# Performance work log

Measured on AMD Instinct MI355X. Metric: run time of the kernel, lower is better.

The kernel has to match this reference:

```python
import jax, jax.numpy as jnp
import numpy as np

BATCH, DIN, HID = 32768, 64, 1024


def setup_inputs() -> dict:
    key = jax.random.key(0)
    ks = jax.random.split(key, 8)
    s_in = 1.0 / np.sqrt(DIN)
    s_h = 1.0 / np.sqrt(HID)
    return {
        "z": jax.random.normal(ks[0], (BATCH, DIN), dtype=jnp.float32),
        # Hamiltonian net: DIN -> HID -> HID -> 1
        "W1": jax.random.normal(ks[1], (DIN, HID), dtype=jnp.float32) * s_in,
        "b1": jnp.zeros((HID,), jnp.float32),
        "W2": jax.random.normal(ks[2], (HID, HID), dtype=jnp.float32) * s_h,
        "b2": jnp.zeros((HID,), jnp.float32),
        "W3": jax.random.normal(ks[3], (HID, 1), dtype=jnp.float32) * s_h,
        "b3": jnp.zeros((1,), jnp.float32),
        # Forcing net: DIN -> HID -> DIN
        "Wf1": jax.random.normal(ks[4], (DIN, HID), dtype=jnp.float32) * s_in,
        "bf1": jnp.zeros((HID,), jnp.float32),
        "Wf2": jax.random.normal(ks[5], (HID, DIN), dtype=jnp.float32) * s_h,
        "bf2": jnp.zeros((DIN,), jnp.float32),
    }


def reference(z, W1, b1, W2, b2, W3, b3, Wf1, bf1, Wf2, bf2):
    def H_sum(zz):
        h1 = jnp.tanh(zz @ W1 + b1)          # [B, HID]
        h2 = jnp.tanh(h1 @ W2 + b2)          # [B, HID]
        return jnp.sum(h2 @ W3 + b3)         # scalar (sum of H over batch)

    gradH = jax.grad(H_sum)(z)               # [B, DIN]
    dim = z.shape[1] // 2
    # symplectic combine: dq/dt = dH/dp, dp/dt = -dH/dq
    hnn_term = jnp.concatenate([gradH[:, dim:], -gradH[:, :dim]], axis=-1)
    forcing_term = jnp.tanh(z @ Wf1 + bf1) @ Wf2 + bf2  # [B, DIN]
    return hnn_term + forcing_term
```

## Files before the change

### kernel.cpp

```cpp
#include <hip/hip_runtime.h>


typedef __attribute__((ext_vector_type(8))) short s16x8;
typedef __attribute__((ext_vector_type(4))) float f32x4;
typedef unsigned short u16;

#define DEVFN static __device__ __forceinline__

constexpr int DIN = 64;
constexpr int HID = 1024;

DEVFN u16 f2bf(float f) {
  unsigned u = __builtin_bit_cast(unsigned, f);
  u += 0x7fffu + ((u >> 16) & 1u);
  return (u16)(u >> 16);
}
DEVFN float bf2f(u16 h) {
  unsigned u = ((unsigned)h) << 16;
  return __builtin_bit_cast(float, u);
}
DEVFN float fast_tanh(float x) {
  float e = __builtin_amdgcn_exp2f(x * 2.8853900817779268f);
  return 1.0f - 2.0f * __builtin_amdgcn_rcpf(e + 1.0f);
}
DEVFN f32x4 mfma16(s16x8 a, s16x8 b, f32x4 c) {
  return __builtin_amdgcn_mfma_f32_16x16x32_bf16(a, b, c, 0, 0, 0);
}

#define GLOAD16(g, l) __builtin_amdgcn_global_load_lds( \
    (const __attribute__((address_space(1))) unsigned int*)(const void*)(g), \
    (__attribute__((address_space(3))) unsigned int*)(void*)(l), 16, 0, 0)

__global__ __launch_bounds__(256) void k0_prep(
    const float* __restrict__ W2, const float* __restrict__ W1,
    const float* __restrict__ Wf1, const float* __restrict__ Wf2,
    u16* __restrict__ W2tp, u16* __restrict__ W2c,
    u16* __restrict__ W1p, u16* __restrict__ Wf1p,
    u16* __restrict__ W1s, u16* __restrict__ Wf2p) {
  __shared__ u16 tl[64 * 65];
  const int bi = blockIdx.x >> 4, bj = blockIdx.x & 15;
  const int tid = threadIdx.x;
#pragma unroll
  for (int i = 0; i < 16; ++i) {
    int idx = i * 256 + tid;
    int r = idx >> 6, c = idx & 63;
    float v = W2[(size_t)(bi * 64 + r) * 1024 + bj * 64 + c];
    u16 b = f2bf(v);
    W2c[(size_t)(bi * 64 + r) * 1024 + bj * 64 + c] = b;
    tl[r * 65 + c] = b;
  }
  __syncthreads();
#pragma unroll
  for (int i = 0; i < 16; ++i) {
    int idx = i * 256 + tid;
    int r = idx >> 6, c = idx & 63;
    W2tp[(size_t)(bj * 64 + r) * 1024 + bi * 64 + c] = tl[c * 65 + r];
  }
  int id = blockIdx.x * 256 + tid;
  int n = id >> 6, k = id & 63;
  W1p[id]  = f2bf(W1[k * HID + n]);
  Wf1p[id] = f2bf(Wf1[k * HID + n]);
  int nn = id >> 10, kk2 = id & 1023;
  float s = (nn < 32) ? 1.f : -1.f;
  W1s[id]  = f2bf(s * W1[((nn + 32) & 63) * HID + kk2]);
  Wf2p[id] = f2bf(Wf2[kk2 * DIN + nn]);
}

__global__ __launch_bounds__(256) void k1_h1(const float* z, const u16* Wp,
                                             const float* b, u16* o) {
  __shared__ __align__(16) u16 zl[64 * 72];
  const int tid = threadIdx.x;
  const int lane = tid & 63, w = tid >> 6;
  const int nb = blockIdx.x & 7, mb = blockIdx.x >> 3;
  const size_t m0 = (size_t)mb * 64;
  const int n0 = nb * 128;
#pragma unroll
  for (int c = 0; c < 4; ++c) {
    int i4 = c * 256 + tid;
    int row = i4 >> 4, col4 = (i4 & 15) * 4;
    f32x4 v = *reinterpret_cast<const f32x4*>(z + (m0 + row) * DIN + col4);
    u16* d = zl + row * 72 + col4;
    d[0] = f2bf(v[0]); d[1] = f2bf(v[1]); d[2] = f2bf(v[2]); d[3] = f2bf(v[3]);
  }
  __syncthreads();
  f32x4 acc[8] = {};
#pragma unroll
  for (int kk = 0; kk < 2; ++kk) {
    const int karr = kk * 32 + ((lane >> 4) << 3);
    s16x8 a = *reinterpret_cast<const s16x8*>(zl + (16 * w + (lane & 15)) * 72 + karr);
#pragma unroll
    for (int fn = 0; fn < 8; ++fn) {
      int n = n0 + fn * 16 + (lane & 15);
      s16x8 bb = *reinterpret_cast<const s16x8*>(Wp + (size_t)n * 64 + karr);
      acc[fn] = mfma16(a, bb, acc[fn]);
    }
  }
#pragma unroll
  for (int fn = 0; fn < 8; ++fn) {
    int n = n0 + fn * 16 + (lane & 15);
    float bias = b[n];
#pragma unroll
    for (int j = 0; j < 4; ++j) {
      size_t m = m0 + 16 * w + ((lane >> 4) << 2) + j;
      o[m * HID + n] = f2bf(fast_tanh(acc[fn][j] + bias));
    }
  }
}

template <int MODE>
__global__ __launch_bounds__(512, 2) void k23_gemm(
    const u16* __restrict__ A, const u16* __restrict__ Bp,
    const float* __restrict__ b2, const float* __restrict__ W3,
    const u16* __restrict__ h1in, u16* __restrict__ outb) {
  extern __shared__ u16 lds[];
  const int tid = threadIdx.x;
  const int lane = tid & 63, w = tid >> 6;
  const int wr = w >> 2, wc = w & 3;
  const int xcd = blockIdx.x & 7, local = blockIdx.x >> 3;
  const size_t m0 = (size_t)(xcd * 16 + (local >> 2)) * 256;
  const int n0 = (local & 3) * 256;

  const u16* gpa[4]; const u16* gpb[4]; int lo[4];
#pragma unroll
  for (int c = 0; c < 4; ++c) {
    int idx = c * 512 + tid, row = idx >> 3, cg = idx & 7;
    int sc = (cg ^ (row & 7)) << 3;
    gpa[c] = A + (m0 + row) * 1024 + sc;
    gpb[c] = Bp + (size_t)(n0 + row) * 1024 + sc;
    lo[c] = idx * 8;
  }
#define STAGE_A(B_, T_) { _Pragma("unroll") for (int c = 0; c < 4; ++c) \
    GLOAD16(gpa[c] + (T_) * 64, lds + (B_) * 32768 + lo[c]); }
#define STAGE_B(B_, T_) { _Pragma("unroll") for (int c = 0; c < 4; ++c) \
    GLOAD16(gpb[c] + (T_) * 64, lds + (B_) * 32768 + 16384 + lo[c]); }

  const int swz = (lane & 7) << 3;
  int aoff[8], boff[4];
#pragma unroll
  for (int i = 0; i < 8; ++i)
    aoff[i] = (wr * 128 + i * 16 + (lane & 15)) * 64 + ((lane >> 4) << 3);
#pragma unroll
  for (int j = 0; j < 4; ++j)
    boff[j] = (wc * 64 + j * 16 + (lane & 15)) * 64 + ((lane >> 4) << 3);

  f32x4 acc[8][4] = {};

#define PHASE(B_, KK_) { \
    s16x8 af[8], bf[4]; \
    _Pragma("unroll") for (int i = 0; i < 8; ++i) \
      af[i] = *reinterpret_cast<const s16x8*>(lds + (B_) * 32768 + ((aoff[i] + (KK_) * 32) ^ swz)); \
    _Pragma("unroll") for (int j = 0; j < 4; ++j) \
      bf[j] = *reinterpret_cast<const s16x8*>(lds + (B_) * 32768 + 16384 + ((boff[j] + (KK_) * 32) ^ swz)); \
    __builtin_amdgcn_s_setprio(1); \
    _Pragma("unroll") for (int i = 0; i < 8; ++i) { \
      _Pragma("unroll") for (int j = 0; j < 4; ++j) \
        acc[i][j] = mfma16(af[i], bf[j], acc[i][j]); } \
    __builtin_amdgcn_s_setprio(0); }

  STAGE_A(0, 0); STAGE_B(0, 0);
  for (int t = 0; t < 15; ++t) {
    const int cur = t & 1, nxt = cur ^ 1;
    STAGE_A(nxt, t + 1);
    asm volatile("s_waitcnt vmcnt(4)" ::: "memory");
    __builtin_amdgcn_s_barrier();
    asm volatile("" ::: "memory");
    PHASE(cur, 0);
    STAGE_B(nxt, t + 1);
    PHASE(cur, 1);
    asm volatile("" ::: "memory");
    __builtin_amdgcn_s_barrier();
    asm volatile("" ::: "memory");
  }
  asm volatile("s_waitcnt vmcnt(0)" ::: "memory");
  __builtin_amdgcn_s_barrier();
  asm volatile("" ::: "memory");
  PHASE(1, 0);
  PHASE(1, 1);
  asm volatile("" ::: "memory");
  __builtin_amdgcn_s_barrier();
  asm volatile("" ::: "memory");

  const int wbase = w * 8192;
  float b2v[4], w3v[4];
  if (MODE == 0) {
#pragma unroll
    for (int j = 0; j < 4; ++j) {
      int n = n0 + wc * 64 + j * 16 + (lane & 15);
      b2v[j] = b2[n]; w3v[j] = W3[n];
    }
  }
#pragma unroll
  for (int h = 0; h < 2; ++h) {
    if (h == 1) asm volatile("s_waitcnt lgkmcnt(0)" ::: "memory");
#pragma unroll
    for (int ip = 0; ip < 4; ++ip) {
#pragma unroll
      for (int j = 0; j < 4; ++j) {
#pragma unroll
        for (int r = 0; r < 4; ++r) {
          float v = acc[h * 4 + ip][j][r];
          u16 o;
          if (MODE == 0) {
            float tt = fast_tanh(v + b2v[j]);
            o = f2bf(w3v[j] * (1.f - tt * tt));
          } else {
            o = f2bf(v);
          }
          int lr = ip * 16 + ((lane >> 4) << 2) + r;
          lds[wbase + lr * 64 + j * 16 + (lane & 15)] = o;
        }
      }
    }
#pragma unroll
    for (int r8 = 0; r8 < 8; ++r8) {
      int lr = r8 * 8 + (lane >> 3), c8 = (lane & 7) * 8;
      s16x8 vv = *reinterpret_cast<const s16x8*>(lds + wbase + lr * 64 + c8);
      size_t grow = m0 + wr * 128 + h * 64 + lr;
      int gcol = n0 + wc * 64 + c8;
      if (MODE == 1) {
        s16x8 hh = *reinterpret_cast<const s16x8*>(h1in + grow * 1024 + gcol);
#pragma unroll
        for (int e = 0; e < 8; ++e) {
          float hv = bf2f((u16)hh[e]);
          vv[e] = (short)f2bf(bf2f((u16)vv[e]) * (1.f - hv * hv));
        }
      }
      *reinterpret_cast<s16x8*>(outb + grow * 1024 + gcol) = vv;
    }
  }
#undef STAGE_A
#undef STAGE_B
#undef PHASE
}

__global__ __launch_bounds__(512) void k4_gemm(
    const u16* __restrict__ gp1, const u16* __restrict__ f1,
    const u16* __restrict__ W1s, const u16* __restrict__ Wf2p,
    const float* __restrict__ bf2, float* __restrict__ out) {
  __shared__ __align__(16) u16 Ab[2][2][4096];
  __shared__ __align__(16) u16 Bb[2][2][4096];
  const int tid = threadIdx.x;
  const int w8 = tid >> 6, lane = tid & 63;
  const int grp = w8 >> 2, w = w8 & 3;
  const int gt = tid & 255;
  const int lr = lane & 15, g = lane >> 4;
  const size_t m0 = (size_t)blockIdx.x * 64;
  const u16* asrc = grp ? f1 : gp1;
  const u16* bsrc = grp ? Wf2p : W1s;

  int aoffs[2], boffs[2], lo[2];
#pragma unroll
  for (int c = 0; c < 2; ++c) {
    int idx = c * 256 + gt;
    int row = idx >> 3, cg = idx & 7;
    aoffs[c] = (int)((m0 + row) * 1024) + ((cg ^ (row & 7)) << 3);
    boffs[c] = row * 1024 + ((cg ^ (row & 7)) << 3);
    lo[c] = idx * 8;
  }
#define K4STAGE(B_, T_) { const int ko_ = (T_) * 64; \
    _Pragma("unroll") for (int c = 0; c < 2; ++c) { \
      GLOAD16(asrc + aoffs[c] + ko_, Ab[grp][B_] + lo[c]); \
      GLOAD16(bsrc + boffs[c] + ko_, Bb[grp][B_] + lo[c]); } }

  const int arow = w * 16 + lr;
  int afr[2], bfr[2][4];
#pragma unroll
  for (int kkl = 0; kkl < 2; ++kkl) {
    afr[kkl] = arow * 64 + ((kkl * 32 + g * 8) ^ ((arow & 7) << 3));
#pragma unroll
    for (int fn = 0; fn < 4; ++fn) {
      int br = fn * 16 + lr;
      bfr[kkl][fn] = br * 64 + ((kkl * 32 + g * 8) ^ ((br & 7) << 3));
    }
  }

  f32x4 acc[4] = {};
#define K4MM(BUF_) { \
    _Pragma("unroll") for (int kkl = 0; kkl < 2; ++kkl) { \
      s16x8 a = *reinterpret_cast<const s16x8*>(Ab[grp][BUF_] + afr[kkl]); \
      _Pragma("unroll") for (int fn = 0; fn < 4; ++fn) { \
        s16x8 b = *reinterpret_cast<const s16x8*>(Bb[grp][BUF_] + bfr[kkl][fn]); \
        acc[fn] = mfma16(a, b, acc[fn]); } } }
#define TBAR() { asm volatile("" ::: "memory"); __builtin_amdgcn_s_barrier(); asm volatile("" ::: "memory"); }

  K4STAGE(0, 0);
  for (int t = 0; t < 15; ++t) {
    K4STAGE((t + 1) & 1, t + 1);
    asm volatile("s_waitcnt vmcnt(4)" ::: "memory");
    TBAR();
    K4MM(t & 1);
    TBAR();
  }
  asm volatile("s_waitcnt vmcnt(0)" ::: "memory");
  TBAR();
  K4MM(1);

  __syncthreads();
  float* red = (float*)&Ab[0][0][0];
  if (grp == 1) {
#pragma unroll
    for (int fn = 0; fn < 4; ++fn)
#pragma unroll
      for (int j = 0; j < 4; ++j)
        red[(fn * 4 + j) * 256 + gt] = acc[fn][j];
  }
  __syncthreads();
  if (grp == 0) {
#pragma unroll
    for (int fn = 0; fn < 4; ++fn) {
      int n = fn * 16 + lr;
      float bias = bf2[n];
#pragma unroll
      for (int j = 0; j < 4; ++j) {
        float v = acc[fn][j] + red[(fn * 4 + j) * 256 + gt] + bias;
        size_t m = m0 + w * 16 + g * 4 + j;
        out[m * DIN + n] = v;
      }
    }
  }
#undef K4STAGE
#undef K4MM
#undef TBAR
}

extern "C" void kernel_launch(void* const* d_in, const int* in_sizes, int n_in,
                              void* d_out, int out_size, void* d_ws, size_t ws_size,
                              hipStream_t stream) {
  const float* z   = (const float*)d_in[0];
  const float* W1  = (const float*)d_in[1];
  const float* b1  = (const float*)d_in[2];
  const float* W2  = (const float*)d_in[3];
  const float* b2  = (const float*)d_in[4];
  const float* W3  = (const float*)d_in[5];
  const float* Wf1 = (const float*)d_in[7];
  const float* bf1 = (const float*)d_in[8];
  const float* Wf2 = (const float*)d_in[9];
  const float* bf2 = (const float*)d_in[10];

  char* ws = (char*)d_ws;
  u16* W1p  = (u16*)(ws + 0);
  u16* Wf1p = (u16*)(ws + 131072);
  u16* W2tp = (u16*)(ws + 262144);
  u16* W2c  = (u16*)(ws + 2359296);
  u16* W1s  = (u16*)(ws + 4456448);
  u16* Wf2p = (u16*)(ws + 4587520);
  u16* h1   = (u16*)(ws + 4718592);
  u16* gp2  = (u16*)(ws + 4718592 + 67108864);
  float* out = (float*)d_out;

  k0_prep<<<256, 256, 0, stream>>>(W2, W1, Wf1, Wf2, W2tp, W2c, W1p, Wf1p, W1s, Wf2p);
  k1_h1<<<4096, 256, 0, stream>>>(z, W1p, b1, h1);
  k23_gemm<0><<<512, 512, 131072, stream>>>(h1, W2tp, b2, W3, nullptr, gp2);
  k23_gemm<1><<<512, 512, 131072, stream>>>(gp2, W2c, nullptr, nullptr, h1, h1);
  k1_h1<<<4096, 256, 0, stream>>>(z, Wf1p, bf1, gp2);
  k4_gemm<<<512, 512, 0, stream>>>(h1, gp2, W1s, Wf2p, bf2, out);
}
```

Measured before the change: 251.5 us.

## Store gp1 and f1 intermediates in 64x64 tiled layout for k4 loads

Adds a tiled 64x64-block layout for the gp1 output of the second k23 GEMM and the forcing hidden activations. When the workspace is large enough, k4 then streams contiguous 8KB tiles per K step instead of strided 128-byte row segments. gp1 goes to a separate buffer. This is meant to improve load locality and DRAM efficiency in k4. The new path depends on workspace size, and the tiled stores from the producers may be less coalesced.

```diff
diff --git a/kernel.cpp b/kernel.cpp
--- a/kernel.cpp
+++ b/kernel.cpp
@@ -25,6 +25,9 @@
 }
 DEVFN f32x4 mfma16(s16x8 a, s16x8 b, f32x4 c) {
   return __builtin_amdgcn_mfma_f32_16x16x32_bf16(a, b, c, 0, 0, 0);
+}
+DEVFN size_t tidx(size_t m, int n) {
+  return (m >> 6) * 65536 + (size_t)(n >> 6) * 4096 + (m & 63) * 64 + (n & 63);
 }
 
 #define GLOAD16(g, l) __builtin_amdgcn_global_load_lds( \
@@ -67,7 +70,7 @@
 }
 
 __global__ __launch_bounds__(256) void k1_h1(const float* z, const u16* Wp,
-                                             const float* b, u16* o) {
+                                             const float* b, u16* o, int tiled) {
   __shared__ __align__(16) u16 zl[64 * 72];
   const int tid = threadIdx.x;
   const int lane = tid & 63, w = tid >> 6;
@@ -102,7 +105,9 @@
 #pragma unroll
     for (int j = 0; j < 4; ++j) {
       size_t m = m0 + 16 * w + ((lane >> 4) << 2) + j;
-      o[m * HID + n] = f2bf(fast_tanh(acc[fn][j] + bias));
+      u16 v = f2bf(fast_tanh(acc[fn][j] + bias));
+      if (tiled) o[tidx(m, n)] = v;
+      else       o[m * HID + n] = v;
     }
   }
 }
@@ -111,7 +116,7 @@
 __global__ __launch_bounds__(512, 2) void k23_gemm(
     const u16* __restrict__ A, const u16* __restrict__ Bp,
     const float* __restrict__ b2, const float* __restrict__ W3,
-    const u16* __restrict__ h1in, u16* __restrict__ outb) {
+    const u16* __restrict__ h1in, u16* __restrict__ outb, int tiled_out) {
   extern __shared__ u16 lds[];
   const int tid = threadIdx.x;
   const int lane = tid & 63, w = tid >> 6;
@@ -225,7 +230,11 @@
           vv[e] = (short)f2bf(bf2f((u16)vv[e]) * (1.f - hv * hv));
         }
       }
-      *reinterpret_cast<s16x8*>(outb + grow * 1024 + gcol) = vv;
+      if (MODE == 1 && tiled_out) {
+        *reinterpret_cast<s16x8*>(outb + tidx(grow, gcol)) = vv;
+      } else {
+        *reinterpret_cast<s16x8*>(outb + grow * 1024 + gcol) = vv;
+      }
     }
   }
 #undef STAGE_A
@@ -236,7 +245,7 @@
 __global__ __launch_bounds__(512) void k4_gemm(
     const u16* __restrict__ gp1, const u16* __restrict__ f1,
     const u16* __restrict__ W1s, const u16* __restrict__ Wf2p,
-    const float* __restrict__ bf2, float* __restrict__ out) {
+    const float* __restrict__ bf2, float* __restrict__ out, int tiled) {
   __shared__ __align__(16) u16 Ab[2][2][4096];
   __shared__ __align__(16) u16 Bb[2][2][4096];
   const int tid = threadIdx.x;
@@ -248,19 +257,22 @@
   const u16* asrc = grp ? f1 : gp1;
   const u16* bsrc = grp ? Wf2p : W1s;
 
-  int aoffs[2], boffs[2], lo[2];
+  size_t aoffs[2]; int boffs[2], lo[2];
+  const int kstep = tiled ? 4096 : 64;
 #pragma unroll
   for (int c = 0; c < 2; ++c) {
     int idx = c * 256 + gt;
     int row = idx >> 3, cg = idx & 7;
-    aoffs[c] = (int)((m0 + row) * 1024) + ((cg ^ (row & 7)) << 3);
-    boffs[c] = row * 1024 + ((cg ^ (row & 7)) << 3);
+    int sc = (cg ^ (row & 7)) << 3;
+    if (tiled) aoffs[c] = (size_t)blockIdx.x * 65536 + row * 64 + sc;
+    else       aoffs[c] = (m0 + row) * 1024 + sc;
+    boffs[c] = row * 1024 + sc;
     lo[c] = idx * 8;
   }
-#define K4STAGE(B_, T_) { const int ko_ = (T_) * 64; \
+#define K4STAGE(B_, T_) { \
     _Pragma("unroll") for (int c = 0; c < 2; ++c) { \
-      GLOAD16(asrc + aoffs[c] + ko_, Ab[grp][B_] + lo[c]); \
-      GLOAD16(bsrc + boffs[c] + ko_, Bb[grp][B_] + lo[c]); } }
+      GLOAD16(asrc + aoffs[c] + (T_) * kstep, Ab[grp][B_] + lo[c]); \
+      GLOAD16(bsrc + boffs[c] + (T_) * 64, Bb[grp][B_] + lo[c]); } }
 
   const int arow = w * 16 + lr;
   int afr[2], bfr[2][4];
@@ -345,13 +357,16 @@
   u16* W1s  = (u16*)(ws + 4456448);
   u16* Wf2p = (u16*)(ws + 4587520);
   u16* h1   = (u16*)(ws + 4718592);
-  u16* gp2  = (u16*)(ws + 4718592 + 67108864);
+  u16* gp2  = (u16*)(ws + 4718592 + 67108864ull);
+  u16* gp1t = (u16*)(ws + 4718592 + 2ull * 67108864ull);
+  const int tiled = ws_size >= (4718592ull + 3ull * 67108864ull) ? 1 : 0;
+  u16* gp1dst = tiled ? gp1t : h1;
   float* out = (float*)d_out;
 
   k0_prep<<<256, 256, 0, stream>>>(W2, W1, Wf1, Wf2, W2tp, W2c, W1p, Wf1p, W1s, Wf2p);
-  k1_h1<<<4096, 256, 0, stream>>>(z, W1p, b1, h1);
-  k23_gemm<0><<<512, 512, 131072, stream>>>(h1, W2tp, b2, W3, nullptr, gp2);
-  k23_gemm<1><<<512, 512, 131072, stream>>>(gp2, W2c, nullptr, nullptr, h1, h1);
-  k1_h1<<<4096, 256, 0, stream>>>(z, Wf1p, bf1, gp2);
-  k4_gemm<<<512, 512, 0, stream>>>(h1, gp2, W1s, Wf2p, bf2, out);
-}
+  k1_h1<<<4096, 256, 0, stream>>>(z, W1p, b1, h1, 0);
+  k23_gemm<0><<<512, 512, 131072, stream>>>(h1, W2tp, b2, W3, nullptr, gp2, 0);
+  k23_gemm<1><<<512, 512, 131072, stream>>>(gp2, W2c, nullptr, nullptr, h1, gp1dst, tiled);
+  k1_h1<<<4096, 256, 0, stream>>>(z, Wf1p, bf1, gp2, tiled);
+  k4_gemm<<<512, 512, 0, stream>>>(gp1dst, gp2, W1s, Wf2p, bf2, out, tiled);
+}
```

After: 265.3 us. +5.5%, slower.

## Fuse dH/dh1 backprop through W1 into second GEMM epilogue with partial sums

Applied to the files above, without the earlier changes.

The second backward GEMM now applies the tanh derivative in LDS and immediately multiplies its 256-column slice by W1, writing fp32 partial gradients per column block. A new final kernel computes only the forcing GEMM and adds the four partials plus bias. This removes the full bf16 write and reread of the gradient activation, at the cost of a 32MB partial buffer, extra LDS round-trips and uncached global B loads inside the epilogue. The fused path runs only if the workspace is large enough.

```diff
diff --git a/kernel.cpp b/kernel.cpp
--- a/kernel.cpp
+++ b/kernel.cpp
@@ -107,11 +107,12 @@
   }
 }
 
-template <int MODE>
+template <int MODE, int FUSE>
 __global__ __launch_bounds__(512, 2) void k23_gemm(
     const u16* __restrict__ A, const u16* __restrict__ Bp,
     const float* __restrict__ b2, const float* __restrict__ W3,
-    const u16* __restrict__ h1in, u16* __restrict__ outb) {
+    const u16* __restrict__ h1in, u16* __restrict__ outb,
+    const u16* __restrict__ W1sg, float* __restrict__ Pbuf) {
   extern __shared__ u16 lds[];
   const int tid = threadIdx.x;
   const int lane = tid & 63, w = tid >> 6;
@@ -177,8 +178,67 @@
   PHASE(1, 0);
   PHASE(1, 1);
   asm volatile("" ::: "memory");
-  __builtin_amdgcn_s_barrier();
-  asm volatile("" ::: "memory");
+  __syncthreads();
+
+  if (MODE == 1 && FUSE) {
+#pragma unroll
+    for (int h = 0; h < 2; ++h)
+#pragma unroll
+      for (int ip = 0; ip < 4; ++ip)
+#pragma unroll
+        for (int j = 0; j < 4; ++j)
+#pragma unroll
+          for (int r = 0; r < 4; ++r) {
+            int rr = wr * 128 + h * 64 + ip * 16 + ((lane >> 4) << 2) + r;
+            int cc = wc * 64 + j * 16 + (lane & 15);
+            lds[rr * 256 + (cc ^ ((rr & 7) << 3))] = f2bf(acc[h * 4 + ip][j][r]);
+          }
+    __syncthreads();
+#pragma unroll
+    for (int c2 = 0; c2 < 16; ++c2) {
+      int idx = c2 * 512 + tid;
+      int r = idx >> 5, cg = (idx & 31) << 3;
+      int ad = r * 256 + (cg ^ ((r & 7) << 3));
+      s16x8 vv = *reinterpret_cast<const s16x8*>(lds + ad);
+      s16x8 hh = *reinterpret_cast<const s16x8*>(h1in + (m0 + r) * 1024 + n0 + cg);
+#pragma unroll
+      for (int e = 0; e < 8; ++e) {
+        float hv = bf2f((u16)hh[e]);
+        vv[e] = (short)f2bf(bf2f((u16)vv[e]) * (1.f - hv * hv));
+      }
+      *reinterpret_cast<s16x8*>(lds + ad) = vv;
+    }
+    __syncthreads();
+    f32x4 acc2[2][4] = {};
+#pragma unroll
+    for (int kk = 0; kk < 8; ++kk) {
+      s16x8 a2[2];
+#pragma unroll
+      for (int fr = 0; fr < 2; ++fr) {
+        int rr = w * 32 + fr * 16 + (lane & 15);
+        int cc = kk * 32 + ((lane >> 4) << 3);
+        a2[fr] = *reinterpret_cast<const s16x8*>(lds + rr * 256 + (cc ^ ((rr & 7) << 3)));
+      }
+#pragma unroll
+      for (int bn = 0; bn < 4; ++bn) {
+        s16x8 b2 = *reinterpret_cast<const s16x8*>(
+            W1sg + (size_t)(bn * 16 + (lane & 15)) * 1024 + n0 + kk * 32 + ((lane >> 4) << 3));
+        acc2[0][bn] = mfma16(a2[0], b2, acc2[0][bn]);
+        acc2[1][bn] = mfma16(a2[1], b2, acc2[1][bn]);
+      }
+    }
+    float* Pp = Pbuf + ((size_t)(xcd * 16 + (local >> 2)) * 4 + (local & 3)) * 16384;
+#pragma unroll
+    for (int fr = 0; fr < 2; ++fr)
+#pragma unroll
+      for (int bn = 0; bn < 4; ++bn)
+#pragma unroll
+        for (int j = 0; j < 4; ++j) {
+          int rr = w * 32 + fr * 16 + ((lane >> 4) << 2) + j;
+          Pp[rr * 64 + bn * 16 + (lane & 15)] = acc2[fr][bn][j];
+        }
+    return;
+  }
 
   const int wbase = w * 8192;
   float b2v[4], w3v[4];
@@ -231,6 +291,86 @@
 #undef STAGE_A
 #undef STAGE_B
 #undef PHASE
+}
+
+__global__ __launch_bounds__(256) void k4f(
+    const u16* __restrict__ f1, const u16* __restrict__ Wf2p,
+    const float* __restrict__ P, const float* __restrict__ bf2,
+    float* __restrict__ out) {
+  __shared__ __align__(16) u16 Ab[2][4096];
+  __shared__ __align__(16) u16 Bb[2][4096];
+  const int tid = threadIdx.x;
+  const int lane = tid & 63, w = tid >> 6;
+  const int lr = lane & 15, g = lane >> 4;
+  const size_t m0 = (size_t)blockIdx.x * 64;
+
+  size_t aoffs[2]; int boffs[2], lo[2];
+#pragma unroll
+  for (int c = 0; c < 2; ++c) {
+    int idx = c * 256 + tid;
+    int row = idx >> 3, cg = idx & 7;
+    int sc = (cg ^ (row & 7)) << 3;
+    aoffs[c] = (m0 + row) * 1024 + sc;
+    boffs[c] = row * 1024 + sc;
+    lo[c] = idx * 8;
+  }
+#define K4STAGE(B_, T_) { \
+    _Pragma("unroll") for (int c = 0; c < 2; ++c) { \
+      GLOAD16(f1 + aoffs[c] + (T_) * 64, Ab[B_] + lo[c]); \
+      GLOAD16(Wf2p + boffs[c] + (T_) * 64, Bb[B_] + lo[c]); } }
+
+  const int arow = w * 16 + lr;
+  int afr[2], bfr[2][4];
+#pragma unroll
+  for (int kkl = 0; kkl < 2; ++kkl) {
+    afr[kkl] = arow * 64 + ((kkl * 32 + g * 8) ^ ((arow & 7) << 3));
+#pragma unroll
+    for (int fn = 0; fn < 4; ++fn) {
+      int br = fn * 16 + lr;
+      bfr[kkl][fn] = br * 64 + ((kkl * 32 + g * 8) ^ ((br & 7) << 3));
+    }
+  }
+
+  f32x4 acc[4] = {};
+#define K4MM(BUF_) { \
+    _Pragma("unroll") for (int kkl = 0; kkl < 2; ++kkl) { \
+      s16x8 a = *reinterpret_cast<const s16x8*>(Ab[BUF_] + afr[kkl]); \
+      _Pragma("unroll") for (int fn = 0; fn < 4; ++fn) { \
+        s16x8 b = *reinterpret_cast<const s16x8*>(Bb[BUF_] + bfr[kkl][fn]); \
+        acc[fn] = mfma16(a, b, acc[fn]); } } }
+#define TBAR() { asm volatile("" ::: "memory"); __builtin_amdgcn_s_barrier(); asm volatile("" ::: "memory"); }
+
+  K4STAGE(0, 0);
+  for (int t = 0; t < 15; ++t) {
+    K4STAGE((t + 1) & 1, t + 1);
+    asm volatile("s_waitcnt vmcnt(4)" ::: "memory");
+    TBAR();
+    K4MM(t & 1);
+    TBAR();
+  }
+  asm volatile("s_waitcnt vmcnt(0)" ::: "memory");
+  TBAR();
+  K4MM(1);
+
+  const int mb = blockIdx.x >> 2, sub = blockIdx.x & 3;
+#pragma unroll
+  for (int fn = 0; fn < 4; ++fn) {
+    int n = fn * 16 + lr;
+    float bias = bf2[n];
+#pragma unroll
+    for (int j = 0; j < 4; ++j) {
+      int rowloc = sub * 64 + w * 16 + g * 4 + j;
+      float s = bias + acc[fn][j];
+#pragma unroll
+      for (int nb = 0; nb < 4; ++nb)
+        s += P[((size_t)mb * 4 + nb) * 16384 + rowloc * 64 + n];
+      size_t m = m0 + w * 16 + g * 4 + j;
+      out[m * DIN + n] = s;
+    }
+  }
+#undef K4STAGE
+#undef K4MM
+#undef TBAR
 }
 
 __global__ __launch_bounds__(512) void k4_gemm(
@@ -345,13 +485,21 @@
   u16* W1s  = (u16*)(ws + 4456448);
   u16* Wf2p = (u16*)(ws + 4587520);
   u16* h1   = (u16*)(ws + 4718592);
-  u16* gp2  = (u16*)(ws + 4718592 + 67108864);
+  u16* gp2  = (u16*)(ws + 4718592 + 67108864ull);
+  float* P  = (float*)(ws + 4718592 + 2ull * 67108864ull);
+  const int fuse = ws_size >= (4718592ull + 2ull * 67108864ull + 33554432ull) ? 1 : 0;
   float* out = (float*)d_out;
 
   k0_prep<<<256, 256, 0, stream>>>(W2, W1, Wf1, Wf2, W2tp, W2c, W1p, Wf1p, W1s, Wf2p);
   k1_h1<<<4096, 256, 0, stream>>>(z, W1p, b1, h1);
-  k23_gemm<0><<<512, 512, 131072, stream>>>(h1, W2tp, b2, W3, nullptr, gp2);
-  k23_gemm<1><<<512, 512, 131072, stream>>>(gp2, W2c, nullptr, nullptr, h1, h1);
-  k1_h1<<<4096, 256, 0, stream>>>(z, Wf1p, bf1, gp2);
-  k4_gemm<<<512, 512, 0, stream>>>(h1, gp2, W1s, Wf2p, bf2, out);
-}
+  k23_gemm<0, 0><<<512, 512, 131072, stream>>>(h1, W2tp, b2, W3, nullptr, gp2, nullptr, nullptr);
+  if (fuse) {
+    k23_gemm<1, 1><<<512, 512, 131072, stream>>>(gp2, W2c, nullptr, nullptr, h1, h1, W1s, P);
+    k1_h1<<<4096, 256, 0, stream>>>(z, Wf1p, bf1, gp2);
+    k4f<<<512, 256, 0, stream>>>(gp2, Wf2p, P, bf2, out);
+  } else {
+    k23_gemm<1, 0><<<512, 512, 131072, stream>>>(gp2, W2c, nullptr, nullptr, h1, h1, nullptr, nullptr);
+    k1_h1<<<4096, 256, 0, stream>>>(z, Wf1p, bf1, gp2);
+    k4_gemm<<<512, 512, 0, stream>>>(h1, gp2, W1s, Wf2p, bf2, out);
+  }
+}
```

After: 260.1 us. 3.4% more time.

## Split final GEMM into split-K partial blocks plus combine kernel

Applied to the files above, without the earlier changes.

The last GEMM is split into four independent blocks per 64-row tile, one per path and K half, each with 256 threads and a single LDS buffer set. Partial sums are written to an fp32 global workspace, and a new combine kernel adds the four partials and the bias. This raises block count and parallelism and removes the in-block LDS reduction. In exchange it adds an extra kernel launch and tens of MB of partial-sum traffic.

```diff
diff --git a/kernel.cpp b/kernel.cpp
--- a/kernel.cpp
+++ b/kernel.cpp
@@ -233,34 +233,36 @@
 #undef PHASE
 }
 
-__global__ __launch_bounds__(512) void k4_gemm(
+__global__ __launch_bounds__(256) void k4_part(
     const u16* __restrict__ gp1, const u16* __restrict__ f1,
     const u16* __restrict__ W1s, const u16* __restrict__ Wf2p,
-    const float* __restrict__ bf2, float* __restrict__ out) {
-  __shared__ __align__(16) u16 Ab[2][2][4096];
-  __shared__ __align__(16) u16 Bb[2][2][4096];
+    float* __restrict__ P4) {
+  __shared__ __align__(16) u16 Ab[2][4096];
+  __shared__ __align__(16) u16 Bb[2][4096];
   const int tid = threadIdx.x;
-  const int w8 = tid >> 6, lane = tid & 63;
-  const int grp = w8 >> 2, w = w8 & 3;
-  const int gt = tid & 255;
+  const int lane = tid & 63, w = tid >> 6;
   const int lr = lane & 15, g = lane >> 4;
-  const size_t m0 = (size_t)blockIdx.x * 64;
-  const u16* asrc = grp ? f1 : gp1;
-  const u16* bsrc = grp ? Wf2p : W1s;
-
-  int aoffs[2], boffs[2], lo[2];
+  const int q = blockIdx.x & 3;
+  const size_t mb = blockIdx.x >> 2;
+  const size_t m0 = mb * 64;
+  const u16* asrc = (q < 2) ? gp1 : f1;
+  const u16* bsrc = (q < 2) ? W1s : Wf2p;
+  const int koff = (q & 1) * 512;
+
+  size_t aoffs[2]; int boffs[2], lo[2];
 #pragma unroll
   for (int c = 0; c < 2; ++c) {
-    int idx = c * 256 + gt;
+    int idx = c * 256 + tid;
     int row = idx >> 3, cg = idx & 7;
-    aoffs[c] = (int)((m0 + row) * 1024) + ((cg ^ (row & 7)) << 3);
-    boffs[c] = row * 1024 + ((cg ^ (row & 7)) << 3);
+    int sc = (cg ^ (row & 7)) << 3;
+    aoffs[c] = (m0 + row) * 1024 + koff + sc;
+    boffs[c] = row * 1024 + koff + sc;
     lo[c] = idx * 8;
   }
-#define K4STAGE(B_, T_) { const int ko_ = (T_) * 64; \
+#define K4STAGE(B_, T_) { \
     _Pragma("unroll") for (int c = 0; c < 2; ++c) { \
-      GLOAD16(asrc + aoffs[c] + ko_, Ab[grp][B_] + lo[c]); \
-      GLOAD16(bsrc + boffs[c] + ko_, Bb[grp][B_] + lo[c]); } }
+      GLOAD16(asrc + aoffs[c] + (T_) * 64, Ab[B_] + lo[c]); \
+      GLOAD16(bsrc + boffs[c] + (T_) * 64, Bb[B_] + lo[c]); } }
 
   const int arow = w * 16 + lr;
   int afr[2], bfr[2][4];
@@ -277,14 +279,14 @@
   f32x4 acc[4] = {};
 #define K4MM(BUF_) { \
     _Pragma("unroll") for (int kkl = 0; kkl < 2; ++kkl) { \
-      s16x8 a = *reinterpret_cast<const s16x8*>(Ab[grp][BUF_] + afr[kkl]); \
+      s16x8 a = *reinterpret_cast<const s16x8*>(Ab[BUF_] + afr[kkl]); \
       _Pragma("unroll") for (int fn = 0; fn < 4; ++fn) { \
-        s16x8 b = *reinterpret_cast<const s16x8*>(Bb[grp][BUF_] + bfr[kkl][fn]); \
+        s16x8 b = *reinterpret_cast<const s16x8*>(Bb[BUF_] + bfr[kkl][fn]); \
         acc[fn] = mfma16(a, b, acc[fn]); } } }
 #define TBAR() { asm volatile("" ::: "memory"); __builtin_amdgcn_s_barrier(); asm volatile("" ::: "memory"); }
 
   K4STAGE(0, 0);
-  for (int t = 0; t < 15; ++t) {
+  for (int t = 0; t < 7; ++t) {
     K4STAGE((t + 1) & 1, t + 1);
     asm volatile("s_waitcnt vmcnt(4)" ::: "memory");
     TBAR();
@@ -295,32 +297,30 @@
   TBAR();
   K4MM(1);
 
-  __syncthreads();
-  float* red = (float*)&Ab[0][0][0];
-  if (grp == 1) {
-#pragma unroll
-    for (int fn = 0; fn < 4; ++fn)
-#pragma unroll
-      for (int j = 0; j < 4; ++j)
-        red[(fn * 4 + j) * 256 + gt] = acc[fn][j];
-  }
-  __syncthreads();
-  if (grp == 0) {
-#pragma unroll
-    for (int fn = 0; fn < 4; ++fn) {
-      int n = fn * 16 + lr;
-      float bias = bf2[n];
-#pragma unroll
-      for (int j = 0; j < 4; ++j) {
-        float v = acc[fn][j] + red[(fn * 4 + j) * 256 + gt] + bias;
-        size_t m = m0 + w * 16 + g * 4 + j;
-        out[m * DIN + n] = v;
-      }
-    }
-  }
+  float* Pp = P4 + (mb * 4 + q) * 4096;
+#pragma unroll
+  for (int fn = 0; fn < 4; ++fn)
+#pragma unroll
+    for (int j = 0; j < 4; ++j)
+      Pp[(w * 16 + g * 4 + j) * 64 + fn * 16 + lr] = acc[fn][j];
 #undef K4STAGE
 #undef K4MM
 #undef TBAR
+}
+
+__global__ __launch_bounds__(256) void k5_combine(
+    const float* __restrict__ P4, const float* __restrict__ bf2,
+    float* __restrict__ out) {
+  int fi = blockIdx.x * 256 + threadIdx.x;
+  int m = fi >> 4, c4 = (fi & 15) * 4;
+  size_t base = (size_t)(m >> 6) * 16384 + (size_t)(m & 63) * 64 + c4;
+  f32x4 s = *reinterpret_cast<const f32x4*>(bf2 + c4);
+#pragma unroll
+  for (int qq = 0; qq < 4; ++qq) {
+    f32x4 p = *reinterpret_cast<const f32x4*>(P4 + base + qq * 4096);
+    s[0] += p[0]; s[1] += p[1]; s[2] += p[2]; s[3] += p[3];
+  }
+  *reinterpret_cast<f32x4*>(out + (size_t)m * 64 + c4) = s;
 }
 
 extern "C" void kernel_launch(void* const* d_in, const int* in_sizes, int n_in,
@@ -345,7 +345,8 @@
   u16* W1s  = (u16*)(ws + 4456448);
   u16* Wf2p = (u16*)(ws + 4587520);
   u16* h1   = (u16*)(ws + 4718592);
-  u16* gp2  = (u16*)(ws + 4718592 + 67108864);
+  u16* gp2  = (u16*)(ws + 4718592 + 67108864ull);
+  float* P4 = (float*)(ws + 4718592 + 2ull * 67108864ull);
   float* out = (float*)d_out;
 
   k0_prep<<<256, 256, 0, stream>>>(W2, W1, Wf1, Wf2, W2tp, W2c, W1p, Wf1p, W1s, Wf2p);
@@ -353,5 +354,6 @@
   k23_gemm<0><<<512, 512, 131072, stream>>>(h1, W2tp, b2, W3, nullptr, gp2);
   k23_gemm<1><<<512, 512, 131072, stream>>>(gp2, W2c, nullptr, nullptr, h1, h1);
   k1_h1<<<4096, 256, 0, stream>>>(z, Wf1p, bf1, gp2);
-  k4_gemm<<<512, 512, 0, stream>>>(h1, gp2, W1s, Wf2p, bf2, out);
-}
+  k4_part<<<2048, 256, 0, stream>>>(h1, gp2, W1s, Wf2p, P4);
+  k5_combine<<<2048, 256, 0, stream>>>(P4, bf2, out);
+}
```

Result: slower. 262.0 us (+4.2%).
